# Optimization experiments

Measured on AMD Instinct MI355X. Metric: run time of the kernel, lower is better.

The kernel has to match this reference:

```python
import jax, jax.numpy as jnp
import numpy as np

B, S, H = 4, 1024, 1024
N_HEADS = 16
HEAD_DIM = H // N_HEADS


def setup_inputs() -> dict:
    key = jax.random.key(0)
    ks = jax.random.split(key, 7)
    scale = 1.0 / np.sqrt(H)
    return {
        "hidden_states": jax.random.normal(ks[0], (B, S, H), dtype=jnp.float32),
        "Wq": jax.random.normal(ks[1], (H, H), dtype=jnp.float32) * scale,
        "bq": jnp.zeros((H,), dtype=jnp.float32),
        "Wk": jax.random.normal(ks[2], (H, H), dtype=jnp.float32) * scale,
        "bk": jnp.zeros((H,), dtype=jnp.float32),
        "Wv": jax.random.normal(ks[3], (H, H), dtype=jnp.float32) * scale,
        "bv": jnp.zeros((H,), dtype=jnp.float32),
    }


def _split_heads(x):
    # [B,S,H] -> [B,h,S,d]
    Bx, Sx, _ = x.shape
    return x.reshape(Bx, Sx, N_HEADS, HEAD_DIM).transpose(0, 2, 1, 3)


def reference(hidden_states, Wq, bq, Wk, bk, Wv, bv):
    q = _split_heads(hidden_states @ Wq + bq)  # [B,h,S,d]
    k = _split_heads(hidden_states @ Wk + bk)
    v = _split_heads(hidden_states @ Wv + bv)
    scores = jnp.einsum("bhqd,bhkd->bhqk", q, k) / jnp.sqrt(
        jnp.asarray(HEAD_DIM, dtype=q.dtype)
    )
    probs = jax.nn.softmax(scores, axis=-1)  # dropout is identity in eval
    ctx = jnp.einsum("bhqk,bhkd->bhqd", probs, v)  # [B,h,S,d]
    return ctx.transpose(0, 2, 1, 3).reshape(B, S, H)
```

## Files before the change

kernel.cpp:

```cpp
#include <hip/hip_runtime.h>
#include <hip/hip_bf16.h>

typedef __bf16 bf16_t;
typedef float f32x4 __attribute__((ext_vector_type(4)));
typedef __bf16 bf16x4 __attribute__((ext_vector_type(4)));
typedef __bf16 bf16x8 __attribute__((ext_vector_type(8)));


__device__ __forceinline__ void g2lds16(const void* g, void* l) {
  __builtin_amdgcn_global_load_lds(
      (const __attribute__((address_space(1))) void*)g,
      (__attribute__((address_space(3))) void*)l, 16, 0, 0);
}

__global__ __launch_bounds__(256) void prep(const float* __restrict__ X,
                                            const float* __restrict__ Wq,
                                            const float* __restrict__ Wk,
                                            const float* __restrict__ Wv,
                                            bf16_t* __restrict__ Xb,
                                            bf16_t* __restrict__ Wtb) {
  __shared__ float tile[32][33];
  if (blockIdx.x < 2048) {
    int i = (blockIdx.x * 256 + threadIdx.x) * 8;
    float4 a = *(const float4*)(X + i);
    float4 b = *(const float4*)(X + i + 4);
    bf16x8 o;
    o[0] = (bf16_t)a.x; o[1] = (bf16_t)a.y; o[2] = (bf16_t)a.z; o[3] = (bf16_t)a.w;
    o[4] = (bf16_t)b.x; o[5] = (bf16_t)b.y; o[6] = (bf16_t)b.z; o[7] = (bf16_t)b.w;
    *(bf16x8*)(Xb + i) = o;
  } else {
    const int bid = blockIdx.x - 2048;
    const int wsel = bid >> 10, bx = bid & 1023;
    const float* W = wsel == 0 ? Wq : (wsel == 1 ? Wk : Wv);
    const int k0 = (bx >> 5) * 32, n0 = (bx & 31) * 32;
    const int tx = threadIdx.x & 31, ty = threadIdx.x >> 5;
#pragma unroll
    for (int i = 0; i < 32; i += 8)
      tile[ty + i][tx] = W[(size_t)(k0 + ty + i) * 1024 + n0 + tx];
    __syncthreads();
#pragma unroll
    for (int i = 0; i < 32; i += 8)
      Wtb[(size_t)(wsel * 1024 + n0 + ty + i) * 1024 + k0 + tx] =
          (bf16_t)tile[tx][ty + i];
  }
}

__global__ __launch_bounds__(256) void gemm_qkv(const bf16_t* __restrict__ Xb,
                                                const bf16_t* __restrict__ Wtb,
                                                const float* __restrict__ bq,
                                                const float* __restrict__ bk,
                                                const float* __restrict__ bv,
                                                bf16_t* __restrict__ Cc,
                                                bf16_t* __restrict__ Vt) {
  __shared__ __align__(16) bf16_t As[128 * 32];
  __shared__ __align__(16) bf16_t Bs[128 * 32];
  const int t = threadIdx.x, lane = t & 63, wave = t >> 6;
  const int g = lane >> 4, r16 = lane & 15;
  const int wg = (blockIdx.x & 7) * 96 + (blockIdx.x >> 3);
  const int tm = wg / 24, tn = wg % 24;
  const int m0 = tm * 128, n0 = tn * 128;
  const bool isV = (n0 >= 2048);
  const int wr = wave >> 1, wc = wave & 1;
  f32x4 zero4 = {0.f, 0.f, 0.f, 0.f};
  f32x4 acc[4][4];
#pragma unroll
  for (int i = 0; i < 4; ++i)
#pragma unroll
    for (int j = 0; j < 4; ++j) acc[i][j] = zero4;
  const int sr = t >> 2, sk = (t & 3) * 8;
  for (int k0 = 0; k0 < 1024; k0 += 32) {
    g2lds16(&Xb[(size_t)(m0 + sr) * 1024 + k0 + sk], (char*)As + wave * 1024);
    g2lds16(&Xb[(size_t)(m0 + 64 + sr) * 1024 + k0 + sk], (char*)As + 4096 + wave * 1024);
    g2lds16(&Wtb[(size_t)(n0 + sr) * 1024 + k0 + sk], (char*)Bs + wave * 1024);
    g2lds16(&Wtb[(size_t)(n0 + 64 + sr) * 1024 + k0 + sk], (char*)Bs + 4096 + wave * 1024);
    __syncthreads();
    bf16x8 af[4], bfr[4];
#pragma unroll
    for (int i = 0; i < 4; ++i)
      af[i] = *(const bf16x8*)&As[(wr * 64 + i * 16 + r16) * 32 + g * 8];
#pragma unroll
    for (int j = 0; j < 4; ++j)
      bfr[j] = *(const bf16x8*)&Bs[(wc * 64 + j * 16 + r16) * 32 + g * 8];
    if (!isV) {
#pragma unroll
      for (int i = 0; i < 4; ++i)
#pragma unroll
        for (int j = 0; j < 4; ++j)
          acc[i][j] = __builtin_amdgcn_mfma_f32_16x16x32_bf16(bfr[j], af[i], acc[i][j], 0, 0, 0);
    } else {
#pragma unroll
      for (int i = 0; i < 4; ++i)
#pragma unroll
        for (int j = 0; j < 4; ++j)
          acc[i][j] = __builtin_amdgcn_mfma_f32_16x16x32_bf16(af[i], bfr[j], acc[i][j], 0, 0, 0);
    }
    __syncthreads();
  }
  if (!isV) {
    const float* barr = (n0 < 1024) ? bq : bk;
    const int bbase = n0 - ((n0 < 1024) ? 0 : 1024) + wc * 64;
    float4 bias4[4];
#pragma unroll
    for (int j = 0; j < 4; ++j)
      bias4[j] = *(const float4*)&barr[bbase + j * 16 + g * 4];
#pragma unroll
    for (int j = 0; j < 4; ++j) {
      const int col0 = n0 + wc * 64 + j * 16 + g * 4;
#pragma unroll
      for (int i = 0; i < 4; ++i) {
        const int row = m0 + wr * 64 + i * 16 + r16;
        bf16x4 o;
        o[0] = (bf16_t)(acc[i][j][0] + bias4[j].x);
        o[1] = (bf16_t)(acc[i][j][1] + bias4[j].y);
        o[2] = (bf16_t)(acc[i][j][2] + bias4[j].z);
        o[3] = (bf16_t)(acc[i][j][3] + bias4[j].w);
        *(bf16x4*)&Cc[(size_t)row * 3072 + col0] = o;
      }
    }
  } else {
#pragma unroll
    for (int j = 0; j < 4; ++j) {
      const int dglob = n0 - 2048 + wc * 64 + j * 16 + r16;
      const float bvj = bv[dglob];
      const int h = dglob >> 6, d = dglob & 63;
#pragma unroll
      for (int i = 0; i < 4; ++i) {
        const int row = m0 + wr * 64 + i * 16 + g * 4;
        const int b = row >> 10, s = row & 1023;
        bf16x4 o;
        o[0] = (bf16_t)(acc[i][j][0] + bvj);
        o[1] = (bf16_t)(acc[i][j][1] + bvj);
        o[2] = (bf16_t)(acc[i][j][2] + bvj);
        o[3] = (bf16_t)(acc[i][j][3] + bvj);
        *(bf16x4*)&Vt[((size_t)(b * 16 + h) * 64 + d) * 1024 + s] = o;
      }
    }
  }
}

__global__ __launch_bounds__(512) void attn_fwd(const bf16_t* __restrict__ Cc,
                                                const bf16_t* __restrict__ Vt,
                                                float* __restrict__ out) {
  __shared__ __align__(16) bf16_t Ks[2][64 * 64];
  __shared__ __align__(16) bf16_t Vts[2][64 * 64];
  __shared__ __align__(16) bf16_t P_lds[8][16][72];
  const int t = threadIdx.x, lane = t & 63, wave = t >> 6;
  const int g = lane >> 4, r16 = lane & 15;
  const int lb = (blockIdx.x & 7) * 64 + (blockIdx.x >> 3);
  const int qb = lb & 7;
  const int bh = lb >> 3;
  const int b = bh >> 4, h = bh & 15;
  const size_t crow0 = (size_t)b * 1024;

  const int qrow = qb * 128 + wave * 16 + r16;
  bf16x8 qf0 = *(const bf16x8*)&Cc[(crow0 + qrow) * 3072 + h * 64 + g * 8];
  bf16x8 qf1 = *(const bf16x8*)&Cc[(crow0 + qrow) * 3072 + h * 64 + 32 + g * 8];

  f32x4 zero4 = {0.f, 0.f, 0.f, 0.f};
  f32x4 ctx[4];
#pragma unroll
  for (int dt = 0; dt < 4; ++dt) ctx[dt] = zero4;
  f32x4 l_lane = zero4;
  const float C2 = 0.125f * 1.44269504f;

  const int kr = t >> 3;
  const int swc = ((t & 7) ^ (kr & 7)) * 8;
  const int ksl0 = (g ^ (r16 & 7)) * 8;
  const int ksl1 = ksl0 ^ 32;
  const bf16_t* Vth = Vt + (size_t)bh * 65536;

  auto stage = [&](int buf, int kt2) {
    const int ks0 = kt2 * 64;
    g2lds16(&Cc[(crow0 + ks0 + kr) * 3072 + 1024 + h * 64 + swc],
            (char*)&Ks[buf][0] + wave * 1024);
    g2lds16(&Vth[(size_t)kr * 1024 + ks0 + swc],
            (char*)&Vts[buf][0] + wave * 1024);
  };

  stage(0, 0);
  __syncthreads();
  int cur = 0;

  for (int kt = 0; kt < 16; ++kt) {
    if (kt < 15) stage(cur ^ 1, kt + 1);

    f32x4 s[4];
#pragma unroll
    for (int jt = 0; jt < 4; ++jt) {
      const bf16_t* kro = &Ks[cur][(jt * 16 + r16) * 64];
      bf16x8 kb0 = *(const bf16x8*)(kro + ksl0);
      bf16x8 kb1 = *(const bf16x8*)(kro + ksl1);
      f32x4 z = __builtin_amdgcn_mfma_f32_16x16x32_bf16(qf0, kb0, zero4, 0, 0, 0);
      s[jt] = __builtin_amdgcn_mfma_f32_16x16x32_bf16(qf1, kb1, z, 0, 0, 0);
    }

#pragma unroll
    for (int jt = 0; jt < 4; ++jt)
#pragma unroll
      for (int r = 0; r < 4; ++r) {
        float pv = exp2f(s[jt][r] * C2);
        l_lane[r] += pv;
        P_lds[wave][g * 4 + r][jt * 16 + r16] = (bf16_t)pv;
      }

    bf16x8 pa0 = *(const bf16x8*)&P_lds[wave][r16][g * 8];
    bf16x8 pa1 = *(const bf16x8*)&P_lds[wave][r16][32 + g * 8];
#pragma unroll
    for (int dt = 0; dt < 4; ++dt) {
      const bf16_t* vro = &Vts[cur][(dt * 16 + r16) * 64];
      bf16x8 vb0 = *(const bf16x8*)(vro + ksl0);
      bf16x8 vb1 = *(const bf16x8*)(vro + ksl1);
      ctx[dt] = __builtin_amdgcn_mfma_f32_16x16x32_bf16(vb0, pa0, ctx[dt], 0, 0, 0);
      ctx[dt] = __builtin_amdgcn_mfma_f32_16x16x32_bf16(vb1, pa1, ctx[dt], 0, 0, 0);
    }
    __syncthreads();
    cur ^= 1;
  }

#pragma unroll
  for (int m = 1; m < 16; m <<= 1)
#pragma unroll
    for (int r = 0; r < 4; ++r) l_lane[r] += __shfl_xor(l_lane[r], m, 64);
  float lr[4];
#pragma unroll
  for (int r = 0; r < 4; ++r) lr[r] = __shfl(l_lane[r], (r16 >> 2) << 4, 64);
  const int rs = r16 & 3;
  const float lden = rs == 0 ? lr[0] : (rs == 1 ? lr[1] : (rs == 2 ? lr[2] : lr[3]));
  const float rinv = 1.0f / lden;

  const int q = qb * 128 + wave * 16 + r16;
#pragma unroll
  for (int dt = 0; dt < 4; ++dt) {
    float4 o = {ctx[dt][0] * rinv, ctx[dt][1] * rinv, ctx[dt][2] * rinv,
                ctx[dt][3] * rinv};
    *(float4*)&out[(crow0 + q) * 1024 + h * 64 + dt * 16 + g * 4] = o;
  }
}

extern "C" void kernel_launch(void* const* d_in, const int* in_sizes, int n_in,
                              void* d_out, int out_size, void* d_ws, size_t ws_size,
                              hipStream_t stream) {
  const float* X  = (const float*)d_in[0];
  const float* Wq = (const float*)d_in[1];
  const float* bq = (const float*)d_in[2];
  const float* Wk = (const float*)d_in[3];
  const float* bk = (const float*)d_in[4];
  const float* Wv = (const float*)d_in[5];
  const float* bv = (const float*)d_in[6];
  float* out = (float*)d_out;
  char* ws = (char*)d_ws;
  bf16_t* Xb  = (bf16_t*)(ws);
  bf16_t* Wtb = (bf16_t*)(ws + 8388608);
  bf16_t* Cc  = (bf16_t*)(ws + 14680064);
  bf16_t* Vt  = (bf16_t*)(ws + 39845888);

  prep<<<5120, 256, 0, stream>>>(X, Wq, Wk, Wv, Xb, Wtb);
  gemm_qkv<<<768, 256, 0, stream>>>(Xb, Wtb, bq, bk, bv, Cc, Vt);
  attn_fwd<<<512, 512, 0, stream>>>(Cc, Vt, out);
}
```

Baseline: 170.1 us.

## Double QKV GEMM K-tile to 64 with XOR-swizzled LDS layout

The QKV projection GEMM now stages 64-wide K slices per iteration instead of 32, halving the number of barrier-separated load/compute rounds. Global-to-LDS loads place chunks at XOR-swizzled positions, and fragment reads apply the matching swizzle to avoid LDS bank conflicts on the wider rows. This doubles shared memory per block, which may reduce occupancy.

New measurement: 161.8 us. 1.05x faster.

```diff
diff --git a/kernel.cpp b/kernel.cpp
--- a/kernel.cpp
+++ b/kernel.cpp
@@ -52,8 +52,8 @@
                                                 const float* __restrict__ bv,
                                                 bf16_t* __restrict__ Cc,
                                                 bf16_t* __restrict__ Vt) {
-  __shared__ __align__(16) bf16_t As[128 * 32];
-  __shared__ __align__(16) bf16_t Bs[128 * 32];
+  __shared__ __align__(16) bf16_t As[128 * 64];
+  __shared__ __align__(16) bf16_t Bs[128 * 64];
   const int t = threadIdx.x, lane = t & 63, wave = t >> 6;
   const int g = lane >> 4, r16 = lane & 15;
   const int wg = (blockIdx.x & 7) * 96 + (blockIdx.x >> 3);
@@ -67,32 +67,45 @@
   for (int i = 0; i < 4; ++i)
 #pragma unroll
     for (int j = 0; j < 4; ++j) acc[i][j] = zero4;
-  const int sr = t >> 2, sk = (t & 3) * 8;
-  for (int k0 = 0; k0 < 1024; k0 += 32) {
-    g2lds16(&Xb[(size_t)(m0 + sr) * 1024 + k0 + sk], (char*)As + wave * 1024);
-    g2lds16(&Xb[(size_t)(m0 + 64 + sr) * 1024 + k0 + sk], (char*)As + 4096 + wave * 1024);
-    g2lds16(&Wtb[(size_t)(n0 + sr) * 1024 + k0 + sk], (char*)Bs + wave * 1024);
-    g2lds16(&Wtb[(size_t)(n0 + 64 + sr) * 1024 + k0 + sk], (char*)Bs + 4096 + wave * 1024);
-    __syncthreads();
-    bf16x8 af[4], bfr[4];
-#pragma unroll
-    for (int i = 0; i < 4; ++i)
-      af[i] = *(const bf16x8*)&As[(wr * 64 + i * 16 + r16) * 32 + g * 8];
-#pragma unroll
-    for (int j = 0; j < 4; ++j)
-      bfr[j] = *(const bf16x8*)&Bs[(wc * 64 + j * 16 + r16) * 32 + g * 8];
-    if (!isV) {
-#pragma unroll
-      for (int i = 0; i < 4; ++i)
-#pragma unroll
-        for (int j = 0; j < 4; ++j)
-          acc[i][j] = __builtin_amdgcn_mfma_f32_16x16x32_bf16(bfr[j], af[i], acc[i][j], 0, 0, 0);
-    } else {
-#pragma unroll
-      for (int i = 0; i < 4; ++i)
-#pragma unroll
-        for (int j = 0; j < 4; ++j)
-          acc[i][j] = __builtin_amdgcn_mfma_f32_16x16x32_bf16(af[i], bfr[j], acc[i][j], 0, 0, 0);
+  const int sr = t >> 3;
+  const int sswz = ((t & 7) ^ (sr & 7)) * 8;
+  const int rsw = r16 & 7;
+
+  for (int k0 = 0; k0 < 1024; k0 += 64) {
+#pragma unroll
+    for (int c = 0; c < 4; ++c) {
+      g2lds16(&Xb[(size_t)(m0 + c * 32 + sr) * 1024 + k0 + sswz],
+              (char*)As + c * 4096 + wave * 1024);
+      g2lds16(&Wtb[(size_t)(n0 + c * 32 + sr) * 1024 + k0 + sswz],
+              (char*)Bs + c * 4096 + wave * 1024);
+    }
+    __syncthreads();
+#pragma unroll
+    for (int kk = 0; kk < 2; ++kk) {
+      bf16x8 af[4], bfr[4];
+#pragma unroll
+      for (int i = 0; i < 4; ++i) {
+        const int ra = wr * 64 + i * 16 + r16;
+        af[i] = *(const bf16x8*)&As[ra * 64 + (((kk * 4 + g) ^ rsw) * 8)];
+      }
+#pragma unroll
+      for (int j = 0; j < 4; ++j) {
+        const int rb = wc * 64 + j * 16 + r16;
+        bfr[j] = *(const bf16x8*)&Bs[rb * 64 + (((kk * 4 + g) ^ rsw) * 8)];
+      }
+      if (!isV) {
+#pragma unroll
+        for (int i = 0; i < 4; ++i)
+#pragma unroll
+          for (int j = 0; j < 4; ++j)
+            acc[i][j] = __builtin_amdgcn_mfma_f32_16x16x32_bf16(bfr[j], af[i], acc[i][j], 0, 0, 0);
+      } else {
+#pragma unroll
+        for (int i = 0; i < 4; ++i)
+#pragma unroll
+          for (int j = 0; j < 4; ++j)
+            acc[i][j] = __builtin_amdgcn_mfma_f32_16x16x32_bf16(af[i], bfr[j], acc[i][j], 0, 0, 0);
+      }
     }
     __syncthreads();
   }
```
